# Kernel optimization log

Measured on AMD Instinct MI355X. Metric: run time of the kernel, lower is better.

The kernel has to match this reference:

```python
import jax, jax.numpy as jnp
import numpy as np

B, N, D = 512, 100000, 64
TAU = 1e-4            # gumbel-softmax temperature from source
SIM_RATIO = 0.5       # similarity_ratio init kwarg
COS_EPS = 1e-6


def setup_inputs() -> dict:
    key = jax.random.key(0)
    k1, k2, k3, k4, k5 = jax.random.split(key, 5)
    need_replace = jax.random.randint(k1, (B, 2), 0, N, dtype=jnp.int64) if jax.config.jax_enable_x64 else jax.random.randint(k1, (B, 2), 0, N, dtype=jnp.int32)
    union_feature = jax.random.normal(k2, (B, 2 * D), dtype=jnp.float32)
    all_items = jax.random.normal(k3, (N, D), dtype=jnp.float32) * 0.1
    W = jax.random.normal(k4, (D, 2 * D), dtype=jnp.float32) * 0.05
    b = jax.random.normal(k5, (D,), dtype=jnp.float32) * 0.01
    return {"need_replace": need_replace, "union_feature": union_feature,
            "all_items": all_items, "W": W, "b": b}


def _cosine(a, b):
    # torch.nn.CosineSimilarity(dim=1, eps=1e-6): dot / max(||a||*||b||, eps)
    dot = jnp.sum(a * b, axis=1)
    na = jnp.linalg.norm(a, axis=1)
    nb = jnp.linalg.norm(b, axis=1)
    return dot / jnp.maximum(na * nb, COS_EPS)


def reference(need_replace, union_feature, all_items, W, b):
    item_ids = need_replace[:, 1]
    items_emb = all_items[item_ids]                      # [B, D]
    uif = union_feature @ W.T + b                        # [B, D] (nn.Linear)
    score = uif @ all_items.T                            # [B, N]

    # gumbel_softmax(tau=1e-4, hard=True), training branch
    g = jax.random.gumbel(jax.random.key(42), score.shape, dtype=score.dtype)
    y_soft = jax.nn.softmax((score + g) / TAU, axis=-1)  # [B, N]
    idx = jnp.argmax(y_soft, axis=-1)                    # [B]
    y_hard = jax.nn.one_hot(idx, N, dtype=score.dtype)
    P = y_hard + y_soft - jax.lax.stop_gradient(y_soft)  # straight-through hard one-hot

    item_sequence = jnp.arange(N, dtype=score.dtype)[None, :]
    replaceable_items = jnp.sum(P * item_sequence, axis=-1).astype(jnp.int32)
    replaceable_feat = P @ all_items                     # [B, D]

    sim = _cosine(items_emb, replaceable_feat)
    sim = (sim + 1.0) / 2.0                              # regularize_similarity
    labels = jnp.full((B,), SIM_RATIO, dtype=sim.dtype)
    similarity_loss = jnp.mean((sim - labels) ** 2)      # SimilarityMarginLoss (assumed MSE-to-margin)
    return replaceable_items, replaceable_feat, similarity_loss, jnp.mean(sim)
```

## Files before the change

### kernel.cpp

```cpp
#include <hip/hip_runtime.h>
#include <cstdint>

#define NITEMS   100000
#define BROWS    512
#define DDIM     64
#define S_BLOCKS 391
#define IPB      256
#define NCHUNKS  782
#define FB_Y     8
#define OUT_FEAT 512
#define OUT_LOSS (512 + 512 * 64)
#define OUT_MSIM (OUT_LOSS + 1)

#define BITS_RAW_T 4284334592u
#define G_TE       6.001f

typedef __attribute__((ext_vector_type(8)))  short  bf16x8;
typedef __attribute__((ext_vector_type(16))) float  f32x16;
typedef unsigned long long u64;
typedef uint32_t u32;

#define ROTL(x, r) __builtin_amdgcn_alignbit((x), (x), 32u - (r))

__device__ __forceinline__ u32 threefry_0_42_xor(u32 e) {
    const u32 K1 = 42u;
    const u32 K2 = 0x1BD11BDAu ^ 42u;
    u32 x0 = 0u;
    u32 x1 = e + K1;
#define TFR(r) { x0 += x1; x1 = ROTL(x1, r) ^ x0; }
    TFR(13u) TFR(15u) TFR(26u) TFR(6u)
    x0 += K1;  x1 += K2 + 1u;
    TFR(17u) TFR(29u) TFR(16u) TFR(24u)
    x0 += K2;  x1 += 2u;
    TFR(13u) TFR(15u) TFR(26u) TFR(6u)
    x1 += K1 + 3u;
    TFR(17u) TFR(29u) TFR(16u) TFR(24u)
    x0 += K1;  x1 += K2 + 4u;
    TFR(13u) TFR(15u) TFR(26u) TFR(6u)
    x0 += K2;  x1 += 5u;
#undef TFR
    return x0 ^ x1;
}

__device__ __forceinline__ float gumbel_from_bits(u32 b) {
    float f = __uint_as_float((b >> 9) | 0x3F800000u) - 1.0f;
    f = fmaxf(f, 1.17549435e-38f);
    return -logf(-logf(f));
}
__device__ __forceinline__ u32 order_map(float v) {
    u32 x = __float_as_uint(v);
    return (x & 0x80000000u) ? ~x : (x | 0x80000000u);
}
__device__ __forceinline__ float unpack_val(u64 p) {
    u32 x = (u32)(p >> 32);
    u32 f = (x & 0x80000000u) ? (x & 0x7FFFFFFFu) : ~x;
    return __uint_as_float(f);
}
__device__ __forceinline__ short f32_to_bf16_rne(float f) {
    u32 b = __float_as_uint(f);
    u32 r = (b + 0x7FFFu + ((b >> 16) & 1u)) >> 16;
    return (short)r;
}
__device__ __forceinline__ float bf16_to_f32(short h) {
    return __uint_as_float(((u32)(uint16_t)h) << 16);
}

__global__ void prep_kernel(const float* __restrict__ UF, const float* __restrict__ W,
                            const float* __restrict__ bias, const float* __restrict__ A,
                            float* __restrict__ uif, float* __restrict__ unorm,
                            float* __restrict__ wsAM4, int* __restrict__ cnt,
                            int* __restrict__ done, float* __restrict__ out) {
    const int t = threadIdx.x, b = blockIdx.x;
    if (b == 0) {
        if (t == 0) { *cnt = 0; out[OUT_LOSS] = 0.f; out[OUT_MSIM] = 0.f; }
        done[t] = 0; done[t + 256] = 0;
    }
    if (b < 128) {
        __shared__ float Wt[128 * 65];
        for (int i = t; i < 8192; i += 256) {
            int d = i >> 7, k = i & 127;
            Wt[k * 65 + d] = W[i];
        }
        __syncthreads();
        const int row = b * 4 + (t >> 6);
        const int d   = t & 63;
        const float* u = UF + row * 128;
        float s = 0.f;
#pragma unroll 4
        for (int k = 0; k < 128; k++) s = fmaf(u[k], Wt[k * 65 + d], s);
        s += bias[d];
        uif[row * 64 + d] = s;
        float q = s * s;
#pragma unroll
        for (int o = 32; o >= 1; o >>= 1) q += __shfl_xor(q, o);
        if (d == 0) unorm[row] = sqrtf(q);
    } else {
        const int item = (b - 128) * 256 + t;
        float q = 0.f;
        if (item < NITEMS) {
            const float4* r = (const float4*)(A + (size_t)item * DDIM);
#pragma unroll
            for (int k = 0; k < 16; k++) {
                float4 x = r[k];
                q = fmaf(x.x, x.x, q); q = fmaf(x.y, x.y, q);
                q = fmaf(x.z, x.z, q); q = fmaf(x.w, x.w, q);
            }
        }
        float n = sqrtf(q);
#pragma unroll
        for (int o = 32; o >= 1; o >>= 1) n = fmaxf(n, __shfl_xor(n, o));
        if ((t & 63) == 0) wsAM4[(b - 128) * 4 + (t >> 6)] = n;
    }
}

__global__ __launch_bounds__(256, 4) void phase1_kernel(
        const float* __restrict__ A, const float* __restrict__ uif,
        u64* __restrict__ wsT1, float* __restrict__ wsB) {
    __shared__ bf16x8 sh_ah[4 * 64];
    __shared__ bf16x8 sh_al[4 * 64];
    const int tid  = threadIdx.x;
    const int lane = tid & 63;
    const int wv   = tid >> 6;
    const int rg   = blockIdx.y;
    const int sb   = blockIdx.x;
    const int itembase = sb * IPB;
    const int ntiles = min(8, (NITEMS - itembase + 31) >> 5);
    const int row   = rg * 128 + wv * 32 + (lane & 31);
    const int khalf = (lane >> 5) * 8;

    bf16x8 uh[4], ul[4];
#pragma unroll
    for (int s = 0; s < 4; s++) {
        const float* src = uif + row * 64 + khalf + 16 * s;
        float4 v0 = *(const float4*)src;
        float4 v1 = *(const float4*)(src + 4);
        float vv[8] = {v0.x, v0.y, v0.z, v0.w, v1.x, v1.y, v1.z, v1.w};
        bf16x8 h, l2;
#pragma unroll
        for (int j = 0; j < 8; j++) {
            short hh = f32_to_bf16_rne(vv[j]);
            float r  = vv[j] - bf16_to_f32(hh);
            h[j] = hh; l2[j] = f32_to_bf16_rne(r);
        }
        uh[s] = h; ul[s] = l2;
    }

    u64 t1p = 0ull; float t1f = -3.0e38f, t2f = -3.0e38f, sm = -3.0e38f;
    const u32 rowbase_e = (u32)row * (u32)NITEMS;

    const int s_i   = tid & 31;
    const int s_c   = tid >> 5;
    const int s_dst = (s_c >> 1) * 64 + s_i + 32 * (s_c & 1);
    const float* s_srcbase = A + (size_t)s_i * 64 + 8 * s_c;

    float4 p0 = *(const float4*)(s_srcbase + (size_t)itembase * 64);
    float4 p1 = *(const float4*)(s_srcbase + (size_t)itembase * 64 + 4);

    for (int t = 0; t < ntiles; t++) {
        const int tb = itembase + t * 32;
        bf16x8 h, l2;
        {
            float vv[8] = {p0.x, p0.y, p0.z, p0.w, p1.x, p1.y, p1.z, p1.w};
#pragma unroll
            for (int j = 0; j < 8; j++) {
                short hh = f32_to_bf16_rne(vv[j]);
                float r  = vv[j] - bf16_to_f32(hh);
                h[j] = hh; l2[j] = f32_to_bf16_rne(r);
            }
        }
        __syncthreads();
        sh_ah[s_dst] = h; sh_al[s_dst] = l2;
        __syncthreads();
        if (t + 1 < ntiles) {
            const float* src = s_srcbase + (size_t)(tb + 32) * 64;
            p0 = *(const float4*)src;
            p1 = *(const float4*)(src + 4);
        }

        f32x16 acc;
#pragma unroll
        for (int z = 0; z < 16; z++) acc[z] = 0.0f;
#pragma unroll
        for (int s = 0; s < 4; s++) {
            bf16x8 ah = sh_ah[s * 64 + lane];
            bf16x8 al = sh_al[s * 64 + lane];
            acc = __builtin_amdgcn_mfma_f32_32x32x16_bf16(ah, uh[s], acc, 0, 0, 0);
            acc = __builtin_amdgcn_mfma_f32_32x32x16_bf16(al, uh[s], acc, 0, 0, 0);
            acc = __builtin_amdgcn_mfma_f32_32x32x16_bf16(ah, ul[s], acc, 0, 0, 0);
        }

        const int ib4 = tb + 4 * (lane >> 5);
#pragma unroll
        for (int i = 0; i < 16; i++) {
            const int il   = (i & 3) + 8 * (i >> 2);
            const int item = ib4 + il;
            u32 rb  = threefry_0_42_xor(rowbase_e + (u32)item);
            float s = acc[i];
            sm = fmaxf(sm, s);
            if (rb >= BITS_RAW_T) {
                float g = gumbel_from_bits(rb);
                float v = s + g;
                if (v > t1f) {
                    t2f = t1f; t1f = v;
                    t1p = ((u64)order_map(v) << 32) | (u32)(~(u32)item);
                } else t2f = fmaxf(t2f, v);
            }
        }
    }

    float bnd = fmaxf(t2f, sm + G_TE);
    {
        u64   op = __shfl_xor(t1p, 32);
        float of = __shfl_xor(t1f, 32);
        float ob = __shfl_xor(bnd, 32);
        if (op > t1p) { bnd = fmaxf(fmaxf(bnd, ob), t1f); t1p = op; t1f = of; }
        else          { bnd = fmaxf(fmaxf(bnd, ob), of); }
    }
    if (lane < 32) {
        wsT1[(size_t)row * S_BLOCKS + sb] = t1p;
        wsB [(size_t)row * S_BLOCKS + sb] = bnd;
    }
}

__global__ void merge_kernel(const u64* __restrict__ wsT1, const float* __restrict__ wsB,
                             const float* __restrict__ wsAM4, const float* __restrict__ unorm,
                             const float* __restrict__ A, const int* __restrict__ need_replace,
                             u64* __restrict__ packed, int* __restrict__ rowlist,
                             int* __restrict__ cnt, float* __restrict__ out) {
    const int row = blockIdx.x, t = threadIdx.x;
    float am = 0.f;
    for (int i = t; i < S_BLOCKS * 4; i += 64) am = fmaxf(am, wsAM4[i]);
    u64 p1 = 0ull; float f1 = -3.0e38f, f2 = -3.0e38f;
    for (int sbk = t; sbk < S_BLOCKS; sbk += 64) {
        u64   ep = wsT1[(size_t)row * S_BLOCKS + sbk];
        float e2 = wsB [(size_t)row * S_BLOCKS + sbk];
        if (ep > p1) { f2 = fmaxf(fmaxf(f1, e2), f2); p1 = ep; f1 = unpack_val(ep); }
        else         { float v = unpack_val(ep); f2 = fmaxf(f2, fmaxf(v, e2)); }
    }
#pragma unroll
    for (int off = 1; off < 64; off <<= 1) {
        u64   op  = __shfl_xor(p1, off);
        float of1 = __shfl_xor(f1, off);
        float of2 = __shfl_xor(f2, off);
        am = fmaxf(am, __shfl_xor(am, off));
        if (op > p1) { f2 = fmaxf(fmaxf(f1, of2), f2); p1 = op; f1 = of1; }
        else         { f2 = fmaxf(f2, fmaxf(of1, of2)); }
    }
    const float E = 1.5e-4f * unorm[row] * am + 3.0e-5f;
    if (f1 - f2 > 2.0f * E) {
        const int idx = (int)(~(u32)(p1 & 0xFFFFFFFFull));
        float fr = A[(size_t)idx * DDIM + t];
        out[OUT_FEAT + row * DDIM + t] = fr;
        int   item = need_replace[2 * row + 1];
        float fa   = A[(size_t)item * DDIM + t];
        float dot = fa * fr, na2 = fa * fa, nb2 = fr * fr;
#pragma unroll
        for (int o = 32; o >= 1; o >>= 1) {
            dot += __shfl_down(dot, o);
            na2 += __shfl_down(na2, o);
            nb2 += __shfl_down(nb2, o);
        }
        if (t == 0) {
            out[row] = (float)idx;
            float denom = fmaxf(sqrtf(na2) * sqrtf(nb2), 1e-6f);
            float sim = (dot / denom + 1.0f) * 0.5f;
            float d = sim - 0.5f;
            atomicAdd(&out[OUT_LOSS], d * d * (1.0f / 512.0f));
            atomicAdd(&out[OUT_MSIM], sim * (1.0f / 512.0f));
        }
    } else if (t == 0) {
        packed[row] = 0ull;
        rowlist[atomicAdd(cnt, 1)] = row;
    }
}

__global__ void fallback_kernel(const float* __restrict__ A, const float* __restrict__ uif,
                                const int* __restrict__ rowlist, const int* __restrict__ cnt,
                                const int* __restrict__ need_replace,
                                u64* __restrict__ packed, int* __restrict__ done,
                                float* __restrict__ out) {
    __shared__ float As[128 * 65];
    __shared__ float Us[64];
    __shared__ int   sh_last;
    const int t  = threadIdx.x;
    const int c  = blockIdx.x;
    const int n0 = c * 128;
    const int nitem = min(128, NITEMS - n0);
    const int total = *cnt;
    if ((int)blockIdx.y >= total) return;

    if (t < nitem) {
        const float4* src = (const float4*)(A + (size_t)(n0 + t) * 64);
#pragma unroll
        for (int k4 = 0; k4 < 16; k4++) {
            float4 x = src[k4];
            As[t * 65 + 4 * k4 + 0] = x.x; As[t * 65 + 4 * k4 + 1] = x.y;
            As[t * 65 + 4 * k4 + 2] = x.z; As[t * 65 + 4 * k4 + 3] = x.w;
        }
    }
    for (int li = blockIdx.y; li < total; li += FB_Y) {
        const int row = rowlist[li];
        __syncthreads();
        if (t < 64) Us[t] = uif[row * 64 + t];
        __syncthreads();
        u64 pk = 0ull;
        if (t < nitem) {
            const int item = n0 + t;
            u32 rb  = threefry_0_42_xor((u32)row * (u32)NITEMS + (u32)item);
            float g = gumbel_from_bits(rb);
            float s0 = 0.f, s1 = 0.f;
#pragma unroll
            for (int k8 = 0; k8 < 64; k8 += 8) {
                s0 = fmaf(As[t * 65 + k8 + 0], Us[k8 + 0], s0);
                s0 = fmaf(As[t * 65 + k8 + 1], Us[k8 + 1], s0);
                s0 = fmaf(As[t * 65 + k8 + 2], Us[k8 + 2], s0);
                s0 = fmaf(As[t * 65 + k8 + 3], Us[k8 + 3], s0);
                s1 = fmaf(As[t * 65 + k8 + 4], Us[k8 + 4], s1);
                s1 = fmaf(As[t * 65 + k8 + 5], Us[k8 + 5], s1);
                s1 = fmaf(As[t * 65 + k8 + 6], Us[k8 + 6], s1);
                s1 = fmaf(As[t * 65 + k8 + 7], Us[k8 + 7], s1);
            }
            float v = (s0 + s1) + g;
            pk = ((u64)order_map(v) << 32) | (u32)(~(u32)item);
        }
#pragma unroll
        for (int off = 1; off < 64; off <<= 1) {
            u64 o = __shfl_xor(pk, off);
            pk = (o > pk) ? o : pk;
        }
        if ((t & 63) == 0) atomicMax(&packed[row], pk);
        __syncthreads();
        if (t == 0) {
            __threadfence();
            sh_last = (atomicAdd(&done[li], 1) == NCHUNKS - 1) ? 1 : 0;
        }
        __syncthreads();
        if (sh_last && t < 64) {
            u64 fin = atomicMax(&packed[row], 0ull);
            const int idx = (int)(~(u32)(fin & 0xFFFFFFFFull));
            float fr = A[(size_t)idx * DDIM + t];
            out[OUT_FEAT + row * DDIM + t] = fr;
            int   item = need_replace[2 * row + 1];
            float fa   = A[(size_t)item * DDIM + t];
            float dot = fa * fr, na2 = fa * fa, nb2 = fr * fr;
#pragma unroll
            for (int o = 32; o >= 1; o >>= 1) {
                dot += __shfl_down(dot, o);
                na2 += __shfl_down(na2, o);
                nb2 += __shfl_down(nb2, o);
            }
            if (t == 0) {
                out[row] = (float)idx;
                float denom = fmaxf(sqrtf(na2) * sqrtf(nb2), 1e-6f);
                float sim = (dot / denom + 1.0f) * 0.5f;
                float d = sim - 0.5f;
                atomicAdd(&out[OUT_LOSS], d * d * (1.0f / 512.0f));
                atomicAdd(&out[OUT_MSIM], sim * (1.0f / 512.0f));
            }
        }
        __syncthreads();
    }
}

extern "C" void kernel_launch(void* const* d_in, const int* in_sizes, int n_in,
                              void* d_out, int out_size, void* d_ws, size_t ws_size,
                              hipStream_t stream) {
    (void)in_sizes; (void)n_in; (void)out_size; (void)ws_size;
    const int*   need_replace = (const int*)d_in[0];
    const float* UF           = (const float*)d_in[1];
    const float* A            = (const float*)d_in[2];
    const float* W            = (const float*)d_in[3];
    const float* bias         = (const float*)d_in[4];
    float* out = (float*)d_out;

    char* ws = (char*)d_ws;
    u64*   wsT1    = (u64*)  (ws);
    float* wsB     = (float*)(ws + 1601536);
    float* uif     = (float*)(ws + 2402304);
    u64*   packed  = (u64*)  (ws + 2533376);
    float* unorm   = (float*)(ws + 2537472);
    float* wsAM4   = (float*)(ws + 2539520);
    int*   rowlist = (int*)  (ws + 2545776);
    int*   cnt     = (int*)  (ws + 2547824);
    int*   done    = (int*)  (ws + 2547828);

    prep_kernel<<<519, 256, 0, stream>>>(UF, W, bias, A, uif, unorm, wsAM4, cnt, done, out);
    phase1_kernel<<<dim3(S_BLOCKS, 4), 256, 0, stream>>>(A, uif, wsT1, wsB);
    merge_kernel<<<BROWS, 64, 0, stream>>>(wsT1, wsB, wsAM4, unorm, A, need_replace,
                                           packed, rowlist, cnt, out);
    fallback_kernel<<<dim3(NCHUNKS, FB_Y), 128, 0, stream>>>(A, uif, rowlist, cnt,
                                                             need_replace, packed, done, out);
}
```

Measured before the change: 260.6 us.

## Pair threefry hashing, raise phase1 occupancy, and shrink fallback grid

Phase1 now hashes two items at once with an interleaved threefry so the two independent dependency chains can hide ALU latency, and its launch bound asks for 6 waves per SIMD instead of 4. The fallback kernel drops the shared-memory staging of item tiles. It now launches 64x8 blocks of 256 threads, each looping over a 1568-item chunk and reading A directly from global memory. This is meant to cut fallback launch and staging overhead when few rows need it, at the cost of longer per-block loops and uncoalesced row reads, and the tighter occupancy bound may cause register spills in phase1.

New measurement: 257.5 us. Within noise of the previous version (-1.2%).

```diff
diff --git a/kernel.cpp b/kernel.cpp
--- a/kernel.cpp
+++ b/kernel.cpp
@@ -6,8 +6,9 @@
 #define DDIM     64
 #define S_BLOCKS 391
 #define IPB      256
-#define NCHUNKS  782
+#define FB_X     64
 #define FB_Y     8
+#define FB_CHUNK 1568
 #define OUT_FEAT 512
 #define OUT_LOSS (512 + 512 * 64)
 #define OUT_MSIM (OUT_LOSS + 1)
@@ -42,6 +43,26 @@
     return x0 ^ x1;
 }
 
+__device__ __forceinline__ void threefry_pair(u32 ea, u32 eb, u32& oa, u32& ob) {
+    const u32 K1 = 42u;
+    const u32 K2 = 0x1BD11BDAu ^ 42u;
+    u32 a0 = 0u, a1 = ea + K1;
+    u32 b0 = 0u, b1 = eb + K1;
+#define TFR2(r) { a0 += a1; b0 += b1; a1 = ROTL(a1, r) ^ a0; b1 = ROTL(b1, r) ^ b0; }
+    TFR2(13u) TFR2(15u) TFR2(26u) TFR2(6u)
+    a0 += K1; a1 += K2 + 1u;  b0 += K1; b1 += K2 + 1u;
+    TFR2(17u) TFR2(29u) TFR2(16u) TFR2(24u)
+    a0 += K2; a1 += 2u;       b0 += K2; b1 += 2u;
+    TFR2(13u) TFR2(15u) TFR2(26u) TFR2(6u)
+    a1 += K1 + 3u;            b1 += K1 + 3u;
+    TFR2(17u) TFR2(29u) TFR2(16u) TFR2(24u)
+    a0 += K1; a1 += K2 + 4u;  b0 += K1; b1 += K2 + 4u;
+    TFR2(13u) TFR2(15u) TFR2(26u) TFR2(6u)
+    a0 += K2; a1 += 5u;       b0 += K2; b1 += 5u;
+#undef TFR2
+    oa = a0 ^ a1; ob = b0 ^ b1;
+}
+
 __device__ __forceinline__ float gumbel_from_bits(u32 b) {
     float f = __uint_as_float((b >> 9) | 0x3F800000u) - 1.0f;
     f = fmaxf(f, 1.17549435e-38f);
@@ -113,7 +134,7 @@
     }
 }
 
-__global__ __launch_bounds__(256, 4) void phase1_kernel(
+__global__ __launch_bounds__(256, 6) void phase1_kernel(
         const float* __restrict__ A, const float* __restrict__ uif,
         u64* __restrict__ wsT1, float* __restrict__ wsB) {
     __shared__ bf16x8 sh_ah[4 * 64];
@@ -191,18 +212,27 @@
 
         const int ib4 = tb + 4 * (lane >> 5);
 #pragma unroll
-        for (int i = 0; i < 16; i++) {
-            const int il   = (i & 3) + 8 * (i >> 2);
-            const int item = ib4 + il;
-            u32 rb  = threefry_0_42_xor(rowbase_e + (u32)item);
-            float s = acc[i];
-            sm = fmaxf(sm, s);
-            if (rb >= BITS_RAW_T) {
-                float g = gumbel_from_bits(rb);
-                float v = s + g;
+        for (int i = 0; i < 16; i += 2) {
+            const int il0 = (i & 3) + 8 * (i >> 2);
+            const int il1 = ((i + 1) & 3) + 8 * ((i + 1) >> 2);
+            const int item0 = ib4 + il0;
+            const int item1 = ib4 + il1;
+            u32 r0, r1;
+            threefry_pair(rowbase_e + (u32)item0, rowbase_e + (u32)item1, r0, r1);
+            float sA = acc[i], sB = acc[i + 1];
+            sm = fmaxf(sm, fmaxf(sA, sB));
+            if (r0 >= BITS_RAW_T) {
+                float v = sA + gumbel_from_bits(r0);
                 if (v > t1f) {
                     t2f = t1f; t1f = v;
-                    t1p = ((u64)order_map(v) << 32) | (u32)(~(u32)item);
+                    t1p = ((u64)order_map(v) << 32) | (u32)(~(u32)item0);
+                } else t2f = fmaxf(t2f, v);
+            }
+            if (r1 >= BITS_RAW_T) {
+                float v = sB + gumbel_from_bits(r1);
+                if (v > t1f) {
+                    t2f = t1f; t1f = v;
+                    t1p = ((u64)order_map(v) << 32) | (u32)(~(u32)item1);
                 } else t2f = fmaxf(t2f, v);
             }
         }
@@ -279,49 +309,40 @@
                                 const int* __restrict__ need_replace,
                                 u64* __restrict__ packed, int* __restrict__ done,
                                 float* __restrict__ out) {
-    __shared__ float As[128 * 65];
     __shared__ float Us[64];
     __shared__ int   sh_last;
     const int t  = threadIdx.x;
-    const int c  = blockIdx.x;
-    const int n0 = c * 128;
-    const int nitem = min(128, NITEMS - n0);
+    const int xb = blockIdx.x;
     const int total = *cnt;
-    if ((int)blockIdx.y >= total) return;
-
-    if (t < nitem) {
-        const float4* src = (const float4*)(A + (size_t)(n0 + t) * 64);
-#pragma unroll
-        for (int k4 = 0; k4 < 16; k4++) {
-            float4 x = src[k4];
-            As[t * 65 + 4 * k4 + 0] = x.x; As[t * 65 + 4 * k4 + 1] = x.y;
-            As[t * 65 + 4 * k4 + 2] = x.z; As[t * 65 + 4 * k4 + 3] = x.w;
-        }
-    }
+    const int iend = min((xb + 1) * FB_CHUNK, NITEMS);
+
     for (int li = blockIdx.y; li < total; li += FB_Y) {
         const int row = rowlist[li];
         __syncthreads();
         if (t < 64) Us[t] = uif[row * 64 + t];
         __syncthreads();
         u64 pk = 0ull;
-        if (t < nitem) {
-            const int item = n0 + t;
+        for (int item = xb * FB_CHUNK + t; item < iend; item += 256) {
             u32 rb  = threefry_0_42_xor((u32)row * (u32)NITEMS + (u32)item);
             float g = gumbel_from_bits(rb);
+            const float4* a4 = (const float4*)(A + (size_t)item * DDIM);
             float s0 = 0.f, s1 = 0.f;
 #pragma unroll
-            for (int k8 = 0; k8 < 64; k8 += 8) {
-                s0 = fmaf(As[t * 65 + k8 + 0], Us[k8 + 0], s0);
-                s0 = fmaf(As[t * 65 + k8 + 1], Us[k8 + 1], s0);
-                s0 = fmaf(As[t * 65 + k8 + 2], Us[k8 + 2], s0);
-                s0 = fmaf(As[t * 65 + k8 + 3], Us[k8 + 3], s0);
-                s1 = fmaf(As[t * 65 + k8 + 4], Us[k8 + 4], s1);
-                s1 = fmaf(As[t * 65 + k8 + 5], Us[k8 + 5], s1);
-                s1 = fmaf(As[t * 65 + k8 + 6], Us[k8 + 6], s1);
-                s1 = fmaf(As[t * 65 + k8 + 7], Us[k8 + 7], s1);
+            for (int k = 0; k < 16; k += 2) {
+                float4 x = a4[k];
+                float4 y = a4[k + 1];
+                s0 = fmaf(x.x, Us[4*k    ], s0);
+                s0 = fmaf(x.y, Us[4*k + 1], s0);
+                s0 = fmaf(x.z, Us[4*k + 2], s0);
+                s0 = fmaf(x.w, Us[4*k + 3], s0);
+                s1 = fmaf(y.x, Us[4*k + 4], s1);
+                s1 = fmaf(y.y, Us[4*k + 5], s1);
+                s1 = fmaf(y.z, Us[4*k + 6], s1);
+                s1 = fmaf(y.w, Us[4*k + 7], s1);
             }
             float v = (s0 + s1) + g;
-            pk = ((u64)order_map(v) << 32) | (u32)(~(u32)item);
+            u64 c = ((u64)order_map(v) << 32) | (u32)(~(u32)item);
+            pk = (c > pk) ? c : pk;
         }
 #pragma unroll
         for (int off = 1; off < 64; off <<= 1) {
@@ -332,7 +353,7 @@
         __syncthreads();
         if (t == 0) {
             __threadfence();
-            sh_last = (atomicAdd(&done[li], 1) == NCHUNKS - 1) ? 1 : 0;
+            sh_last = (atomicAdd(&done[li], 1) == FB_X - 1) ? 1 : 0;
         }
         __syncthreads();
         if (sh_last && t < 64) {
@@ -388,6 +409,6 @@
     phase1_kernel<<<dim3(S_BLOCKS, 4), 256, 0, stream>>>(A, uif, wsT1, wsB);
     merge_kernel<<<BROWS, 64, 0, stream>>>(wsT1, wsB, wsAM4, unorm, A, need_replace,
                                            packed, rowlist, cnt, out);
-    fallback_kernel<<<dim3(NCHUNKS, FB_Y), 128, 0, stream>>>(A, uif, rowlist, cnt,
-                                                             need_replace, packed, done, out);
-}
+    fallback_kernel<<<dim3(FB_X, FB_Y), 256, 0, stream>>>(A, uif, rowlist, cnt,
+                                                          need_replace, packed, done, out);
+}
```
